# Performance work log

Hardware: AMD Instinct MI355X
Metric: run time of the kernel (lower is better)

## Reference

```python
import jax, jax.numpy as jnp
import numpy as np

ENC_IN = 64
D_MODEL = 512
B, T = 256, 256


def setup_inputs() -> dict:
    key = jax.random.key(0)
    ks = jax.random.split(key, 16)
    d = D_MODEL
    std = 1.0 / np.sqrt(d)
    def w(k, shape):
        return jax.random.normal(k, shape, dtype=jnp.float32) * std
    return {
        'x': jax.random.normal(ks[0], (B, T, ENC_IN), dtype=jnp.float32),
        'Wa': w(ks[1], (d, 2 * d)),
        'Ua': w(ks[2], (d, 2 * d)),
        'ba': jnp.zeros((2 * d,), jnp.float32),
        'Wna': w(ks[3], (d, d)),
        'Una': w(ks[4], (d, d)),
        'bna': jnp.zeros((d,), jnp.float32),
        'WAttn': w(ks[5], (d, d)),
        'UAttn': w(ks[6], (d, d)),
        'VAttn': w(ks[7], (d, d)),
        'Wma': w(ks[8], (d, d)),
        'Uma': w(ks[9], (d, d)),
        'bma': jax.random.normal(ks[10], (d,), dtype=jnp.float32),  # bias init torch.randn, dim==1 so not re-initialized
        'Wm': w(ks[11], (ENC_IN, 2 * d)),
        'Um': w(ks[12], (d, 2 * d)),
        'bm': jnp.zeros((2 * d,), jnp.float32),
        'Whm': w(ks[13], (ENC_IN, d)),
        'Uhm': w(ks[14], (d, d)),
        'bhm': jnp.zeros((d,), jnp.float32),
    }


def reference(x, Wa, Ua, ba, Wna, Una, bna, WAttn, UAttn, VAttn,
              Wma, Uma, bma, Wm, Um, bm, Whm, Uhm, bhm):
    Bsz = x.shape[0]
    H = Wna.shape[0]

    def step(carry, x_t):
        h, N, h_pp = carry           # h = h_{t-1}, h_pp = h_{t-2}
        d_t = h - h_pp               # 0 at t=0, h_0 at t=1, diff otherwise
        gates_A = d_t @ Wa + N @ Ua + ba
        z_A = jax.nn.sigmoid(gates_A[:, :H])
        r_A = jax.nn.sigmoid(gates_A[:, H:])
        hat_N = jnp.tanh(d_t @ Wna + (N * r_A) @ Una + bna)
        N_new = (1.0 - z_A) * N + z_A * hat_N
        score = jnp.tanh(h @ WAttn + N_new @ UAttn) @ VAttn
        alpha = jax.nn.softmax(score, axis=1)
        Omega = alpha * N_new
        m = jnp.tanh(Omega @ Wma + h @ Uma + bma)
        gates_M = x_t @ Wm + m @ Um + bm
        z_M = jax.nn.sigmoid(gates_M[:, :H])
        r_M = jax.nn.sigmoid(gates_M[:, H:])
        hat_h = jnp.tanh(x_t @ Whm + (m * r_M) @ Uhm + bhm)
        h_new = (1.0 - z_M) * h + z_M * hat_h
        return (h_new, N_new, h), h_new

    h0 = jnp.zeros((Bsz, H), x.dtype)
    init = (h0, h0, h0)
    (h_T, N_T, _), hs = jax.lax.scan(step, init, jnp.swapaxes(x, 0, 1))  # hs: [T,B,H]
    hidden_seq = jnp.swapaxes(hs, 0, 1)  # [B,T,H]
    return hidden_seq, (h_T, N_T)
```

## Files before the change

### kernel.cpp

```cpp
#include <hip/hip_runtime.h>

static constexpr int Bsz  = 256;
static constexpr int Tseq = 256;
static constexpr int Hd   = 512;
static constexpr int Ein  = 64;
static constexpr int NBLK = 256;
static constexpr int NTHR = 512;

typedef __attribute__((ext_vector_type(8))) short bf16x8;
typedef __attribute__((ext_vector_type(4))) float f32x4;
typedef __attribute__((ext_vector_type(8))) _Float16 f16x8;
typedef unsigned long long u64;

__device__ __forceinline__ float sigm(float x) { return 1.f / (1.f + expf(-x)); }
__device__ __forceinline__ short f2bf(float f) {
  union { float f; unsigned u; } v; v.f = f;
  unsigned r = v.u + 0x7FFFu + ((v.u >> 16) & 1u);
  return (short)(r >> 16);
}
__device__ __forceinline__ float bf2f(short s) {
  union { float f; unsigned u; } v; v.u = ((unsigned)(unsigned short)s) << 16; return v.f;
}

__device__ __forceinline__ void llc_ld8h(f16x8& d, const _Float16* p) {
  asm volatile("global_load_dwordx4 %0, %1, off sc0 sc1" : "=v"(d) : "v"(p));
}
__device__ __forceinline__ void llc_sth(_Float16* p, _Float16 v) {
  asm volatile("global_store_short %0, %1, off sc0 sc1" :: "v"(p), "v"(v) : "memory");
}
__device__ __forceinline__ void vwait() {
  asm volatile("s_waitcnt vmcnt(0)" ::: "memory");
  __builtin_amdgcn_sched_barrier(0);
}

struct KP {
  const float *x, *ba, *bna, *bma, *bm, *bhm;
  const short *Wh[13], *Wl[13];
  _Float16 *Hbuf, *Nst, *NrA, *s1, *score, *mbuf, *mrM;
  float* out;
  unsigned* cnt;
};

__global__ __launch_bounds__(256)
void prepack(const float* __restrict__ W, short* __restrict__ Whi,
             short* __restrict__ Wlo, int N)
{
  __shared__ float lds[32][257];
  const int tid = threadIdx.x;
  const int k0 = blockIdx.y * 32;
  const int n0 = blockIdx.x * 256;
  #pragma unroll
  for (int i = 0; i < 8; ++i) {
    const int flat = (i * 256 + tid) * 4;
    const int r = flat >> 8, c = flat & 255;
    const float4 v = *(const float4*)(W + (size_t)(k0 + r) * N + n0 + c);
    lds[r][c] = v.x; lds[r][c + 1] = v.y; lds[r][c + 2] = v.z; lds[r][c + 3] = v.w;
  }
  __syncthreads();
  const int lane = tid & 63, wv = tid >> 6;
  const int kr = (lane >> 4) * 8;
  const int cc = lane & 15;
  for (int nt = wv; nt < 16; nt += 4) {
    const int ntg = (n0 >> 4) + nt;
    const size_t off = ((size_t)((k0 >> 5) * (N >> 4) + ntg) * 64 + lane) * 8;
    bf16x8 vh, vl;
    #pragma unroll
    for (int j = 0; j < 8; ++j) {
      const float v = lds[kr + j][nt * 16 + cc];
      const short hb = f2bf(v);
      vh[j] = hb; vl[j] = f2bf(v - bf2f(hb));
    }
    *(bf16x8*)(Whi + off) = vh;
    *(bf16x8*)(Wlo + off) = vl;
  }
}

__device__ __forceinline__ void task_write(int task, f32x4 u0, f32x4 u1,
                                           short* hi, short* lo) {
  const int o = task << 3;
  bf16x8 vh, vl;
  #pragma unroll
  for (int j = 0; j < 4; ++j) {
    const short h0 = f2bf(u0[j]); vh[j]     = h0; vl[j]     = f2bf(u0[j] - bf2f(h0));
    const short h1 = f2bf(u1[j]); vh[j + 4] = h1; vl[j + 4] = f2bf(u1[j] - bf2f(h1));
  }
  *(bf16x8*)(hi + o) = vh;
  *(bf16x8*)(lo + o) = vl;
}
__device__ __forceinline__ void h2f8(f16x8 v, f32x4& a0, f32x4& a1) {
  #pragma unroll
  for (int j = 0; j < 4; ++j) { a0[j] = (float)v[j]; a1[j] = (float)v[j + 4]; }
}

__device__ __forceinline__ void stageSlice(const _Float16* src, short* hi, short* lo,
                                           int wid, int lane) {
  f16x8 a, b;
  llc_ld8h(a, src + (wid << 9) + (lane << 3));
  llc_ld8h(b, src + ((wid + 8) << 9) + (lane << 3));
  vwait();
  const int tb = ((lane >> 2) << 6) | ((lane & 3) << 4);
  f32x4 a0, a1, b0, b1;
  h2f8(a, a0, a1); h2f8(b, b0, b1);
  task_write(tb | wid, a0, a1, hi, lo);
  task_write(tb | (wid + 8), b0, b1, hi, lo);
}

__device__ __forceinline__ void mm(const short* Ah, const short* Al,
                                   const short* __restrict__ Wh,
                                   const short* __restrict__ Wl,
                                   int ntN, int ntg, int kc0, int kc1,
                                   int lane, f32x4& acc)
{
  for (int kc = kc0; kc < kc1; ++kc) {
    const int ao = ((kc << 6) | lane) << 3;
    const bf16x8 ah = *(const bf16x8*)(Ah + ao);
    const bf16x8 al = *(const bf16x8*)(Al + ao);
    const size_t o = ((size_t)((kc * ntN + ntg) << 6 | lane)) << 3;
    const bf16x8 bh = *(const bf16x8*)(Wh + o);
    const bf16x8 bl = *(const bf16x8*)(Wl + o);
    acc = __builtin_amdgcn_mfma_f32_16x16x32_bf16(ah, bh, acc, 0, 0, 0);
    acc = __builtin_amdgcn_mfma_f32_16x16x32_bf16(al, bh, acc, 0, 0, 0);
    acc = __builtin_amdgcn_mfma_f32_16x16x32_bf16(ah, bl, acc, 0, 0, 0);
  }
}

__device__ __forceinline__ void gbar(unsigned* cnt, int stripe, unsigned& ph) {
  asm volatile("s_waitcnt vmcnt(0)" ::: "memory");
  __syncthreads();
  ++ph;
  if (threadIdx.x == 0) {
    __hip_atomic_fetch_add(&cnt[stripe << 4], 1u, __ATOMIC_RELAXED,
                           __HIP_MEMORY_SCOPE_AGENT);
    const unsigned tgt = ph * 16u;
    while (__hip_atomic_load(&cnt[stripe << 4], __ATOMIC_RELAXED,
                             __HIP_MEMORY_SCOPE_AGENT) < tgt)
      __builtin_amdgcn_s_sleep(4);
  }
  __syncthreads();
}

__global__ __launch_bounds__(NTHR, 1)
void dtgru(KP P)
{
  __shared__ short sAh[8192], sAl[8192];
  __shared__ short sBh[8192], sBl[8192];
  __shared__ short sCh[8192], sCl[8192];
  __shared__ short sDh[8192], sDl[8192];
  __shared__ short sXh[1024], sXl[1024];
  __shared__ float red[2048];
  const int tid = threadIdx.x, lane = tid & 63, wid = tid >> 6;
  const int bid = blockIdx.x;
  const int g = bid & 15;
  const int stripe = bid >> 4;
  const int r0 = stripe << 4;
  const int nt = wid & 1;
  const int q  = wid >> 1;
  const int mat  = (wid >> 1) & 1;
  const int half = wid >> 2;
  const int ntb = (g << 1) | nt;
  const int col5 = (g << 5) | (nt << 4) | (lane & 15);
  const int rb = r0 + ((lane >> 4) << 2);
  unsigned ph = 0;
  float Nreg[4] = {0,0,0,0}, hreg[4] = {0,0,0,0};
  float zAreg[4] = {0,0,0,0}, zMreg[4] = {0,0,0,0}, mreg[4] = {0,0,0,0};
  const float b_az = P.ba[col5],  b_ar = P.ba[col5 + 512];
  const float b_na = P.bna[col5], b_ma = P.bma[col5];
  const float b_mz = P.bm[col5],  b_mr = P.bm[col5 + 512];
  const float b_hm = P.bhm[col5];

  for (int i = tid; i < 2048; i += NTHR) {
    ((u64*)sBh)[i] = 0; ((u64*)sBl)[i] = 0;
    ((u64*)sDh)[i] = 0; ((u64*)sDl)[i] = 0;
  }
  __syncthreads();

  #pragma clang loop unroll(disable)
  for (int t = 0; t < Tseq; ++t) {
    {
      const _Float16* Hr = P.Hbuf + (r0 << 9);
      f16x8 ha, hb;
      llc_ld8h(ha, Hr + (wid << 9) + (lane << 3));
      llc_ld8h(hb, Hr + ((wid + 8) << 9) + (lane << 3));
      f32x4 x0 = {0,0,0,0}, x1 = {0,0,0,0};
      if (tid < 128) {
        const float* px = P.x + ((size_t)(r0 + (tid >> 3)) * Tseq + t) * Ein
                        + ((tid & 7) << 3);
        x0 = *(const f32x4*)px; x1 = *(const f32x4*)(px + 4);
      }
      vwait();
      const int tb = ((lane >> 2) << 6) | ((lane & 3) << 4);
      auto p1w = [&](int task, f16x8 hv) {
        const int o = task << 3;
        f32x4 u0, u1; h2f8(hv, u0, u1);
        const bf16x8 dh = *(const bf16x8*)(sDh + o), dlo = *(const bf16x8*)(sDl + o);
        f32x4 d0, d1;
        #pragma unroll
        for (int j = 0; j < 4; ++j) {
          d0[j] = u0[j] - (bf2f(dh[j])     + bf2f(dlo[j]));
          d1[j] = u1[j] - (bf2f(dh[j + 4]) + bf2f(dlo[j + 4]));
        }
        task_write(task, d0, d1, sAh, sAl);
        task_write(task, u0, u1, sDh, sDl);
      };
      p1w(tb | wid, ha);
      p1w(tb | (wid + 8), hb);
      if (tid < 128) {
        const int tx = (((tid & 7) >> 2) << 6) | (tid >> 3) | ((tid & 3) << 4);
        task_write(tx, x0, x1, sXh, sXl);
      }
    }
    __syncthreads();
    {
      f32x4 acc = {0,0,0,0};
      const int ntg = (half ? 32 : 0) | ((g << 1) | nt);
      if (!mat) mm(sAh, sAl, P.Wh[0], P.Wl[0], 64, ntg, 0, 16, lane, acc);
      else      mm(sBh, sBl, P.Wh[1], P.Wl[1], 64, ntg, 0, 16, lane, acc);
      if (mat) *(f32x4*)&red[(((half << 1) | nt) << 8) | (lane << 2)] = acc;
      __syncthreads();
      if (!mat) acc += *(f32x4*)&red[(((half << 1) | nt) << 8) | (lane << 2)];
      __syncthreads();
      if (!mat && half) *(f32x4*)&red[(nt << 8) | (lane << 2)] = acc;
      __syncthreads();
      if (!mat && !half) {
        const f32x4 ar = *(const f32x4*)&red[(nt << 8) | (lane << 2)];
        #pragma unroll
        for (int i = 0; i < 4; ++i) {
          zAreg[i] = sigm(acc[i] + b_az);
          const float rA = sigm(ar[i] + b_ar);
          llc_sth(&P.NrA[((rb + i) << 9) | col5], (_Float16)(Nreg[i] * rA));
        }
      }
    }
    gbar(P.cnt, stripe, ph);

    stageSlice(P.NrA + (r0 << 9), sBh, sBl, wid, lane);
    __syncthreads();
    {
      f32x4 acc = {0,0,0,0};
      const int kc0 = (q & 1) << 3;
      if (!(q >> 1)) mm(sAh, sAl, P.Wh[2], P.Wl[2], 32, ntb, kc0, kc0 + 8, lane, acc);
      else           mm(sBh, sBl, P.Wh[3], P.Wl[3], 32, ntb, kc0, kc0 + 8, lane, acc);
      if (q) *(f32x4*)&red[((((q - 1) << 1) | nt) << 8) | (lane << 2)] = acc;
      __syncthreads();
      if (!q) {
        #pragma unroll
        for (int j = 0; j < 3; ++j) acc += *(f32x4*)&red[(((j << 1) | nt) << 8) | (lane << 2)];
        #pragma unroll
        for (int i = 0; i < 4; ++i) {
          const float hn = tanhf(acc[i] + b_na);
          const float Nn = (1.f - zAreg[i]) * Nreg[i] + zAreg[i] * hn;
          Nreg[i] = Nn;
          llc_sth(&P.Nst[((rb + i) << 9) | col5], (_Float16)Nn);
        }
      }
    }
    gbar(P.cnt, stripe, ph);

    stageSlice(P.Nst + (r0 << 9), sBh, sBl, wid, lane);
    __syncthreads();
    {
      f32x4 acc = {0,0,0,0};
      const int kc0 = (q & 1) << 3;
      if (!(q >> 1)) mm(sDh, sDl, P.Wh[4], P.Wl[4], 32, ntb, kc0, kc0 + 8, lane, acc);
      else           mm(sBh, sBl, P.Wh[5], P.Wl[5], 32, ntb, kc0, kc0 + 8, lane, acc);
      if (q) *(f32x4*)&red[((((q - 1) << 1) | nt) << 8) | (lane << 2)] = acc;
      __syncthreads();
      if (!q) {
        #pragma unroll
        for (int j = 0; j < 3; ++j) acc += *(f32x4*)&red[(((j << 1) | nt) << 8) | (lane << 2)];
        #pragma unroll
        for (int i = 0; i < 4; ++i)
          llc_sth(&P.s1[((rb + i) << 9) | col5], (_Float16)tanhf(acc[i]));
      }
    }
    gbar(P.cnt, stripe, ph);

    stageSlice(P.s1 + (r0 << 9), sCh, sCl, wid, lane);
    __syncthreads();
    {
      f32x4 acc = {0,0,0,0};
      mm(sCh, sCl, P.Wh[6], P.Wl[6], 32, ntb, q << 2, (q << 2) + 4, lane, acc);
      if (q) *(f32x4*)&red[((((q - 1) << 1) | nt) << 8) | (lane << 2)] = acc;
      __syncthreads();
      if (!q) {
        #pragma unroll
        for (int j = 0; j < 3; ++j) acc += *(f32x4*)&red[(((j << 1) | nt) << 8) | (lane << 2)];
        #pragma unroll
        for (int i = 0; i < 4; ++i)
          llc_sth(&P.score[((rb + i) << 9) | col5], (_Float16)acc[i]);
      }
    }
    gbar(P.cnt, stripe, ph);

    {
      const int lr0 = wid << 1;
      f16x8 s0v, s1v;
      llc_ld8h(s0v, P.score + ((r0 + lr0) << 9) + (lane << 3));
      llc_ld8h(s1v, P.score + ((r0 + lr0 + 1) << 9) + (lane << 3));
      vwait();
      #pragma unroll
      for (int rr = 0; rr < 2; ++rr) {
        const int lr = lr0 | rr;
        f32x4 v0, v1; h2f8(rr ? s1v : s0v, v0, v1);
        float mx = v0[0];
        #pragma unroll
        for (int j = 1; j < 4; ++j) mx = fmaxf(mx, v0[j]);
        #pragma unroll
        for (int j = 0; j < 4; ++j) mx = fmaxf(mx, v1[j]);
        #pragma unroll
        for (int d = 1; d < 64; d <<= 1) mx = fmaxf(mx, __shfl_xor(mx, d));
        float e[8];
        #pragma unroll
        for (int j = 0; j < 4; ++j) { e[j] = expf(v0[j] - mx); e[j + 4] = expf(v1[j] - mx); }
        float sm = ((e[0] + e[1]) + (e[2] + e[3])) + ((e[4] + e[5]) + (e[6] + e[7]));
        #pragma unroll
        for (int d = 1; d < 64; d <<= 1) sm += __shfl_xor(sm, d);
        const float inv = 1.f / sm;
        const int o = (((lane >> 2) << 6) | lr | ((lane & 3) << 4)) << 3;
        const bf16x8 nh = *(const bf16x8*)(sBh + o), nl = *(const bf16x8*)(sBl + o);
        bf16x8 vh, vl;
        #pragma unroll
        for (int j = 0; j < 8; ++j) {
          const float om = e[j] * inv * (bf2f(nh[j]) + bf2f(nl[j]));
          const short hb = f2bf(om);
          vh[j] = hb; vl[j] = f2bf(om - bf2f(hb));
        }
        *(bf16x8*)(sCh + o) = vh;
        *(bf16x8*)(sCl + o) = vl;
      }
    }
    __syncthreads();
    {
      f32x4 acc = {0,0,0,0};
      const int kc0 = (q & 1) << 3;
      if (!(q >> 1)) mm(sCh, sCl, P.Wh[7], P.Wl[7], 32, ntb, kc0, kc0 + 8, lane, acc);
      else           mm(sDh, sDl, P.Wh[8], P.Wl[8], 32, ntb, kc0, kc0 + 8, lane, acc);
      if (q) *(f32x4*)&red[((((q - 1) << 1) | nt) << 8) | (lane << 2)] = acc;
      __syncthreads();
      if (!q) {
        #pragma unroll
        for (int j = 0; j < 3; ++j) acc += *(f32x4*)&red[(((j << 1) | nt) << 8) | (lane << 2)];
        #pragma unroll
        for (int i = 0; i < 4; ++i) {
          const float m = tanhf(acc[i] + b_ma);
          mreg[i] = m;
          llc_sth(&P.mbuf[((rb + i) << 9) | col5], (_Float16)m);
        }
      }
    }
    gbar(P.cnt, stripe, ph);

    stageSlice(P.mbuf + (r0 << 9), sAh, sAl, wid, lane);
    __syncthreads();
    {
      f32x4 acc = {0,0,0,0};
      const int ntg = (half ? 32 : 0) | ((g << 1) | nt);
      if (!mat) { mm(sXh, sXl, P.Wh[9],  P.Wl[9],  64, ntg, 0, 2, lane, acc);
                  mm(sAh, sAl, P.Wh[10], P.Wl[10], 64, ntg, 0, 7, lane, acc); }
      else      { mm(sAh, sAl, P.Wh[10], P.Wl[10], 64, ntg, 7, 16, lane, acc); }
      if (mat) *(f32x4*)&red[(((half << 1) | nt) << 8) | (lane << 2)] = acc;
      __syncthreads();
      if (!mat) acc += *(f32x4*)&red[(((half << 1) | nt) << 8) | (lane << 2)];
      __syncthreads();
      if (!mat && half) *(f32x4*)&red[(nt << 8) | (lane << 2)] = acc;
      __syncthreads();
      if (!mat && !half) {
        const f32x4 ar = *(const f32x4*)&red[(nt << 8) | (lane << 2)];
        #pragma unroll
        for (int i = 0; i < 4; ++i) {
          zMreg[i] = sigm(acc[i] + b_mz);
          const float rM = sigm(ar[i] + b_mr);
          llc_sth(&P.mrM[((rb + i) << 9) | col5], (_Float16)(mreg[i] * rM));
        }
      }
    }
    gbar(P.cnt, stripe, ph);

    stageSlice(P.mrM + (r0 << 9), sCh, sCl, wid, lane);
    __syncthreads();
    {
      f32x4 acc = {0,0,0,0};
      if (q == 0)      { mm(sXh, sXl, P.Wh[11], P.Wl[11], 32, ntb, 0, 2, lane, acc);
                         mm(sCh, sCl, P.Wh[12], P.Wl[12], 32, ntb, 0, 2, lane, acc); }
      else if (q == 1)   mm(sCh, sCl, P.Wh[12], P.Wl[12], 32, ntb, 2, 7, lane, acc);
      else if (q == 2)   mm(sCh, sCl, P.Wh[12], P.Wl[12], 32, ntb, 7, 12, lane, acc);
      else               mm(sCh, sCl, P.Wh[12], P.Wl[12], 32, ntb, 12, 16, lane, acc);
      if (q) *(f32x4*)&red[((((q - 1) << 1) | nt) << 8) | (lane << 2)] = acc;
      __syncthreads();
      if (!q) {
        #pragma unroll
        for (int j = 0; j < 3; ++j) acc += *(f32x4*)&red[(((j << 1) | nt) << 8) | (lane << 2)];
        #pragma unroll
        for (int i = 0; i < 4; ++i) {
          const float hh = tanhf(acc[i] + b_hm);
          const float hn = (1.f - zMreg[i]) * hreg[i] + zMreg[i] * hh;
          hreg[i] = hn;
          llc_sth(&P.Hbuf[((rb + i) << 9) | col5], (_Float16)hn);
          P.out[((((size_t)(rb + i)) << 8 | t) << 9) | col5] = hn;
        }
      }
    }
    gbar(P.cnt, stripe, ph);
  }
}

__global__ __launch_bounds__(256)
void initk(_Float16* hbuf, unsigned* cnt) {
  const int i = blockIdx.x * 256 + threadIdx.x;
  hbuf[i] = (_Float16)0.f;
  if (blockIdx.x == 0) cnt[threadIdx.x] = 0u;
}

__global__ __launch_bounds__(256)
void finalize(const _Float16* __restrict__ hT, const _Float16* __restrict__ nT,
              float* __restrict__ oh, float* __restrict__ on) {
  const int i = blockIdx.x * 256 + threadIdx.x;
  unsigned a, b;
  asm volatile("global_load_ushort %0, %1, off sc0 sc1" : "=v"(a) : "v"(&hT[i]));
  asm volatile("global_load_ushort %0, %1, off sc0 sc1" : "=v"(b) : "v"(&nT[i]));
  vwait();
  unsigned short ua = (unsigned short)a, ub = (unsigned short)b;
  _Float16 ha, hb;
  __builtin_memcpy(&ha, &ua, 2); __builtin_memcpy(&hb, &ub, 2);
  oh[i] = (float)ha; on[i] = (float)hb;
}

extern "C" void kernel_launch(void* const* d_in, const int* in_sizes, int n_in,
                              void* d_out, int out_size, void* d_ws, size_t ws_size,
                              hipStream_t stream)
{
  (void)in_sizes; (void)n_in; (void)out_size; (void)ws_size;

  unsigned* cnt = (unsigned*)d_ws;
  _Float16* hw = (_Float16*)((unsigned*)d_ws + 256);
  const int S = Bsz * Hd;

  KP P{};
  P.x   = (const float*)d_in[0];
  P.ba  = (const float*)d_in[3];
  P.bna = (const float*)d_in[6];
  P.bma = (const float*)d_in[12];
  P.bm  = (const float*)d_in[15];
  P.bhm = (const float*)d_in[18];
  P.Hbuf = hw;          P.Nst = hw + S;      P.NrA = hw + 2 * S;
  P.s1   = hw + 3 * S;  P.score = hw + 4 * S;
  P.mbuf = hw + 5 * S;  P.mrM = hw + 6 * S;
  P.out = (float*)d_out;
  P.cnt = cnt;
  float* out_hT = P.out + (size_t)Bsz * Tseq * Hd;
  float* out_NT = out_hT + S;

  short* wpk = (short*)(hw + 7 * S);
  const int widx[13] = {1, 2, 4, 5, 7, 8, 9, 10, 11, 13, 14, 16, 17};
  const int wK[13]   = {512, 512, 512, 512, 512, 512, 512, 512, 512, 64, 512, 64, 512};
  const int wN[13]   = {1024, 1024, 512, 512, 512, 512, 512, 512, 512, 1024, 1024, 512, 512};
  {
    size_t off = 0;
    for (int i = 0; i < 13; ++i) {
      const size_t sz = (size_t)wK[i] * wN[i];
      P.Wh[i] = wpk + off; off += sz;
      P.Wl[i] = wpk + off; off += sz;
    }
  }
  for (int i = 0; i < 13; ++i) {
    dim3 gg(wN[i] / 256, wK[i] / 32);
    prepack<<<gg, 256, 0, stream>>>((const float*)d_in[widx[i]],
                                    (short*)P.Wh[i], (short*)P.Wl[i], wN[i]);
  }

  initk<<<S / 256, 256, 0, stream>>>(P.Hbuf, cnt);

  dtgru<<<NBLK, NTHR, 0, stream>>>(P);

  finalize<<<S / 256, 256, 0, stream>>>(P.Hbuf, P.Nst, out_hT, out_NT);
}
```

Before: 18.19 ms.

## Halve rows per block and double grid to 512 persistent blocks

Each block now processes 8 batch rows instead of 16, so the grid doubles to 512 blocks (32 stripes of 16), and launch bounds allow several blocks per CU. Shared memory is merged into one array and its size shrinks. Upper MFMA rows read a zero region, and stores from those rows are masked. The aim is more parallelism and more blocks resident per CU for the latency-bound recurrent loop. In exchange, half of each MFMA is wasted on padding, weight reads per useful row double, and twice as many stripe barriers are needed.

```diff
diff --git a/kernel.cpp b/kernel.cpp
--- a/kernel.cpp
+++ b/kernel.cpp
@@ -4,13 +4,17 @@
 static constexpr int Tseq = 256;
 static constexpr int Hd   = 512;
 static constexpr int Ein  = 64;
-static constexpr int NBLK = 256;
+static constexpr int NBLK = 512;
 static constexpr int NTHR = 512;
 
 typedef __attribute__((ext_vector_type(8))) short bf16x8;
 typedef __attribute__((ext_vector_type(4))) float f32x4;
 typedef __attribute__((ext_vector_type(8))) _Float16 f16x8;
 typedef unsigned long long u64;
+
+static constexpr int OAh = 0,     OBh = 8192,  OCh = 16384, ODh = 24576;
+static constexpr int OXh = 32768, OZ = 33792;
+static constexpr int SSZ = 34304;
 
 __device__ __forceinline__ float sigm(float x) { return 1.f / (1.f + expf(-x)); }
 __device__ __forceinline__ short f2bf(float f) {
@@ -75,46 +79,45 @@
   }
 }
 
-__device__ __forceinline__ void task_write(int task, f32x4 u0, f32x4 u1,
-                                           short* hi, short* lo) {
-  const int o = task << 3;
+__device__ __forceinline__ int to8(int r, int lane) {
+  return ((((lane >> 2) << 5) | r | ((lane & 3) << 3)) << 3);
+}
+__device__ __forceinline__ void task_write8(short* S, int base, int lo, int o,
+                                            f32x4 u0, f32x4 u1) {
   bf16x8 vh, vl;
   #pragma unroll
   for (int j = 0; j < 4; ++j) {
     const short h0 = f2bf(u0[j]); vh[j]     = h0; vl[j]     = f2bf(u0[j] - bf2f(h0));
     const short h1 = f2bf(u1[j]); vh[j + 4] = h1; vl[j + 4] = f2bf(u1[j] - bf2f(h1));
   }
-  *(bf16x8*)(hi + o) = vh;
-  *(bf16x8*)(lo + o) = vl;
+  *(bf16x8*)(S + base + o) = vh;
+  *(bf16x8*)(S + base + lo + o) = vl;
 }
 __device__ __forceinline__ void h2f8(f16x8 v, f32x4& a0, f32x4& a1) {
   #pragma unroll
   for (int j = 0; j < 4; ++j) { a0[j] = (float)v[j]; a1[j] = (float)v[j + 4]; }
 }
 
-__device__ __forceinline__ void stageSlice(const _Float16* src, short* hi, short* lo,
-                                           int wid, int lane) {
-  f16x8 a, b;
+__device__ __forceinline__ void stageSlice(short* S, int base,
+                                           const _Float16* src, int wid, int lane) {
+  f16x8 a;
   llc_ld8h(a, src + (wid << 9) + (lane << 3));
-  llc_ld8h(b, src + ((wid + 8) << 9) + (lane << 3));
   vwait();
-  const int tb = ((lane >> 2) << 6) | ((lane & 3) << 4);
-  f32x4 a0, a1, b0, b1;
-  h2f8(a, a0, a1); h2f8(b, b0, b1);
-  task_write(tb | wid, a0, a1, hi, lo);
-  task_write(tb | (wid + 8), b0, b1, hi, lo);
-}
-
-__device__ __forceinline__ void mm(const short* Ah, const short* Al,
+  f32x4 a0, a1; h2f8(a, a0, a1);
+  task_write8(S, base, 4096, to8(wid, lane), a0, a1);
+}
+
+__device__ __forceinline__ void mm(const short* S, int abase, int lo,
                                    const short* __restrict__ Wh,
                                    const short* __restrict__ Wl,
                                    int ntN, int ntg, int kc0, int kc1,
                                    int lane, f32x4& acc)
 {
+  const bool zr = (lane & 8) != 0;
   for (int kc = kc0; kc < kc1; ++kc) {
-    const int ao = ((kc << 6) | lane) << 3;
-    const bf16x8 ah = *(const bf16x8*)(Ah + ao);
-    const bf16x8 al = *(const bf16x8*)(Al + ao);
+    const int rel = (((kc << 5) | (lane & 7) | ((lane >> 4) << 3)) << 3);
+    const bf16x8 ah = *(const bf16x8*)(S + (zr ? OZ : abase + rel));
+    const bf16x8 al = *(const bf16x8*)(S + (zr ? OZ : abase + lo + rel));
     const size_t o = ((size_t)((kc * ntN + ntg) << 6 | lane)) << 3;
     const bf16x8 bh = *(const bf16x8*)(Wh + o);
     const bf16x8 bl = *(const bf16x8*)(Wl + o);
@@ -139,20 +142,16 @@
   __syncthreads();
 }
 
-__global__ __launch_bounds__(NTHR, 1)
+__global__ __launch_bounds__(NTHR, 4)
 void dtgru(KP P)
 {
-  __shared__ short sAh[8192], sAl[8192];
-  __shared__ short sBh[8192], sBl[8192];
-  __shared__ short sCh[8192], sCl[8192];
-  __shared__ short sDh[8192], sDl[8192];
-  __shared__ short sXh[1024], sXl[1024];
-  __shared__ float red[2048];
+  __shared__ short S[SSZ];
+  __shared__ float red[1536];
   const int tid = threadIdx.x, lane = tid & 63, wid = tid >> 6;
   const int bid = blockIdx.x;
   const int g = bid & 15;
   const int stripe = bid >> 4;
-  const int r0 = stripe << 4;
+  const int r0 = stripe << 3;
   const int nt = wid & 1;
   const int q  = wid >> 1;
   const int mat  = (wid >> 1) & 1;
@@ -160,6 +159,7 @@
   const int ntb = (g << 1) | nt;
   const int col5 = (g << 5) | (nt << 4) | (lane & 15);
   const int rb = r0 + ((lane >> 4) << 2);
+  const bool rowok = lane < 32;
   unsigned ph = 0;
   float Nreg[4] = {0,0,0,0}, hreg[4] = {0,0,0,0};
   float zAreg[4] = {0,0,0,0}, zMreg[4] = {0,0,0,0}, mreg[4] = {0,0,0,0};
@@ -168,53 +168,47 @@
   const float b_mz = P.bm[col5],  b_mr = P.bm[col5 + 512];
   const float b_hm = P.bhm[col5];
 
-  for (int i = tid; i < 2048; i += NTHR) {
-    ((u64*)sBh)[i] = 0; ((u64*)sBl)[i] = 0;
-    ((u64*)sDh)[i] = 0; ((u64*)sDl)[i] = 0;
-  }
+  for (int i = tid; i < SSZ / 4; i += NTHR) ((u64*)S)[i] = 0;
   __syncthreads();
 
   #pragma clang loop unroll(disable)
   for (int t = 0; t < Tseq; ++t) {
     {
       const _Float16* Hr = P.Hbuf + (r0 << 9);
-      f16x8 ha, hb;
+      f16x8 ha;
       llc_ld8h(ha, Hr + (wid << 9) + (lane << 3));
-      llc_ld8h(hb, Hr + ((wid + 8) << 9) + (lane << 3));
       f32x4 x0 = {0,0,0,0}, x1 = {0,0,0,0};
-      if (tid < 128) {
+      if (tid < 64) {
         const float* px = P.x + ((size_t)(r0 + (tid >> 3)) * Tseq + t) * Ein
                         + ((tid & 7) << 3);
         x0 = *(const f32x4*)px; x1 = *(const f32x4*)(px + 4);
       }
       vwait();
-      const int tb = ((lane >> 2) << 6) | ((lane & 3) << 4);
-      auto p1w = [&](int task, f16x8 hv) {
-        const int o = task << 3;
-        f32x4 u0, u1; h2f8(hv, u0, u1);
-        const bf16x8 dh = *(const bf16x8*)(sDh + o), dlo = *(const bf16x8*)(sDl + o);
+      {
+        const int o = to8(wid, lane);
+        f32x4 u0, u1; h2f8(ha, u0, u1);
+        const bf16x8 dh = *(const bf16x8*)(S + ODh + o);
+        const bf16x8 dl = *(const bf16x8*)(S + ODh + 4096 + o);
         f32x4 d0, d1;
         #pragma unroll
         for (int j = 0; j < 4; ++j) {
-          d0[j] = u0[j] - (bf2f(dh[j])     + bf2f(dlo[j]));
-          d1[j] = u1[j] - (bf2f(dh[j + 4]) + bf2f(dlo[j + 4]));
-        }
-        task_write(task, d0, d1, sAh, sAl);
-        task_write(task, u0, u1, sDh, sDl);
-      };
-      p1w(tb | wid, ha);
-      p1w(tb | (wid + 8), hb);
-      if (tid < 128) {
-        const int tx = (((tid & 7) >> 2) << 6) | (tid >> 3) | ((tid & 3) << 4);
-        task_write(tx, x0, x1, sXh, sXl);
+          d0[j] = u0[j] - (bf2f(dh[j])     + bf2f(dl[j]));
+          d1[j] = u1[j] - (bf2f(dh[j + 4]) + bf2f(dl[j + 4]));
+        }
+        task_write8(S, OAh, 4096, o, d0, d1);
+        task_write8(S, ODh, 4096, o, u0, u1);
+      }
+      if (tid < 64) {
+        const int ox = (((((tid >> 2) & 1) << 5) | (tid >> 3) | ((tid & 3) << 3)) << 3);
+        task_write8(S, OXh, 512, ox, x0, x1);
       }
     }
     __syncthreads();
     {
       f32x4 acc = {0,0,0,0};
       const int ntg = (half ? 32 : 0) | ((g << 1) | nt);
-      if (!mat) mm(sAh, sAl, P.Wh[0], P.Wl[0], 64, ntg, 0, 16, lane, acc);
-      else      mm(sBh, sBl, P.Wh[1], P.Wl[1], 64, ntg, 0, 16, lane, acc);
+      if (!mat) mm(S, OAh, 4096, P.Wh[0], P.Wl[0], 64, ntg, 0, 16, lane, acc);
+      else      mm(S, OBh, 4096, P.Wh[1], P.Wl[1], 64, ntg, 0, 16, lane, acc);
       if (mat) *(f32x4*)&red[(((half << 1) | nt) << 8) | (lane << 2)] = acc;
       __syncthreads();
       if (!mat) acc += *(f32x4*)&red[(((half << 1) | nt) << 8) | (lane << 2)];
@@ -227,19 +221,19 @@
         for (int i = 0; i < 4; ++i) {
           zAreg[i] = sigm(acc[i] + b_az);
           const float rA = sigm(ar[i] + b_ar);
-          llc_sth(&P.NrA[((rb + i) << 9) | col5], (_Float16)(Nreg[i] * rA));
-        }
-      }
-    }
-    gbar(P.cnt, stripe, ph);
-
-    stageSlice(P.NrA + (r0 << 9), sBh, sBl, wid, lane);
+          if (rowok) llc_sth(&P.NrA[((rb + i) << 9) | col5], (_Float16)(Nreg[i] * rA));
+        }
+      }
+    }
+    gbar(P.cnt, stripe, ph);
+
+    stageSlice(S, OBh, P.NrA + (r0 << 9), wid, lane);
     __syncthreads();
     {
       f32x4 acc = {0,0,0,0};
       const int kc0 = (q & 1) << 3;
-      if (!(q >> 1)) mm(sAh, sAl, P.Wh[2], P.Wl[2], 32, ntb, kc0, kc0 + 8, lane, acc);
-      else           mm(sBh, sBl, P.Wh[3], P.Wl[3], 32, ntb, kc0, kc0 + 8, lane, acc);
+      if (!(q >> 1)) mm(S, OAh, 4096, P.Wh[2], P.Wl[2], 32, ntb, kc0, kc0 + 8, lane, acc);
+      else           mm(S, OBh, 4096, P.Wh[3], P.Wl[3], 32, ntb, kc0, kc0 + 8, lane, acc);
       if (q) *(f32x4*)&red[((((q - 1) << 1) | nt) << 8) | (lane << 2)] = acc;
       __syncthreads();
       if (!q) {
@@ -250,19 +244,19 @@
           const float hn = tanhf(acc[i] + b_na);
           const float Nn = (1.f - zAreg[i]) * Nreg[i] + zAreg[i] * hn;
           Nreg[i] = Nn;
-          llc_sth(&P.Nst[((rb + i) << 9) | col5], (_Float16)Nn);
-        }
-      }
-    }
-    gbar(P.cnt, stripe, ph);
-
-    stageSlice(P.Nst + (r0 << 9), sBh, sBl, wid, lane);
+          if (rowok) llc_sth(&P.Nst[((rb + i) << 9) | col5], (_Float16)Nn);
+        }
+      }
+    }
+    gbar(P.cnt, stripe, ph);
+
+    stageSlice(S, OBh, P.Nst + (r0 << 9), wid, lane);
     __syncthreads();
     {
       f32x4 acc = {0,0,0,0};
       const int kc0 = (q & 1) << 3;
-      if (!(q >> 1)) mm(sDh, sDl, P.Wh[4], P.Wl[4], 32, ntb, kc0, kc0 + 8, lane, acc);
-      else           mm(sBh, sBl, P.Wh[5], P.Wl[5], 32, ntb, kc0, kc0 + 8, lane, acc);
+      if (!(q >> 1)) mm(S, ODh, 4096, P.Wh[4], P.Wl[4], 32, ntb, kc0, kc0 + 8, lane, acc);
+      else           mm(S, OBh, 4096, P.Wh[5], P.Wl[5], 32, ntb, kc0, kc0 + 8, lane, acc);
       if (q) *(f32x4*)&red[((((q - 1) << 1) | nt) << 8) | (lane << 2)] = acc;
       __syncthreads();
       if (!q) {
@@ -270,16 +264,16 @@
         for (int j = 0; j < 3; ++j) acc += *(f32x4*)&red[(((j << 1) | nt) << 8) | (lane << 2)];
         #pragma unroll
         for (int i = 0; i < 4; ++i)
-          llc_sth(&P.s1[((rb + i) << 9) | col5], (_Float16)tanhf(acc[i]));
-      }
-    }
-    gbar(P.cnt, stripe, ph);
-
-    stageSlice(P.s1 + (r0 << 9), sCh, sCl, wid, lane);
-    __syncthreads();
-    {
-      f32x4 acc = {0,0,0,0};
-      mm(sCh, sCl, P.Wh[6], P.Wl[6], 32, ntb, q << 2, (q << 2) + 4, lane, acc);
+          if (rowok) llc_sth(&P.s1[((rb + i) << 9) | col5], (_Float16)tanhf(acc[i]));
+      }
+    }
+    gbar(P.cnt, stripe, ph);
+
+    stageSlice(S, OCh, P.s1 + (r0 << 9), wid, lane);
+    __syncthreads();
+    {
+      f32x4 acc = {0,0,0,0};
+      mm(S, OCh, 4096, P.Wh[6], P.Wl[6], 32, ntb, q << 2, (q << 2) + 4, lane, acc);
       if (q) *(f32x4*)&red[((((q - 1) << 1) | nt) << 8) | (lane << 2)] = acc;
       __syncthreads();
       if (!q) {
@@ -287,54 +281,47 @@
         for (int j = 0; j < 3; ++j) acc += *(f32x4*)&red[(((j << 1) | nt) << 8) | (lane << 2)];
         #pragma unroll
         for (int i = 0; i < 4; ++i)
-          llc_sth(&P.score[((rb + i) << 9) | col5], (_Float16)acc[i]);
-      }
-    }
-    gbar(P.cnt, stripe, ph);
-
-    {
-      const int lr0 = wid << 1;
-      f16x8 s0v, s1v;
-      llc_ld8h(s0v, P.score + ((r0 + lr0) << 9) + (lane << 3));
-      llc_ld8h(s1v, P.score + ((r0 + lr0 + 1) << 9) + (lane << 3));
+          if (rowok) llc_sth(&P.score[((rb + i) << 9) | col5], (_Float16)acc[i]);
+      }
+    }
+    gbar(P.cnt, stripe, ph);
+
+    {
+      f16x8 sv;
+      llc_ld8h(sv, P.score + ((r0 + wid) << 9) + (lane << 3));
       vwait();
-      #pragma unroll
-      for (int rr = 0; rr < 2; ++rr) {
-        const int lr = lr0 | rr;
-        f32x4 v0, v1; h2f8(rr ? s1v : s0v, v0, v1);
-        float mx = v0[0];
-        #pragma unroll
-        for (int j = 1; j < 4; ++j) mx = fmaxf(mx, v0[j]);
-        #pragma unroll
-        for (int j = 0; j < 4; ++j) mx = fmaxf(mx, v1[j]);
-        #pragma unroll
-        for (int d = 1; d < 64; d <<= 1) mx = fmaxf(mx, __shfl_xor(mx, d));
-        float e[8];
-        #pragma unroll
-        for (int j = 0; j < 4; ++j) { e[j] = expf(v0[j] - mx); e[j + 4] = expf(v1[j] - mx); }
-        float sm = ((e[0] + e[1]) + (e[2] + e[3])) + ((e[4] + e[5]) + (e[6] + e[7]));
-        #pragma unroll
-        for (int d = 1; d < 64; d <<= 1) sm += __shfl_xor(sm, d);
-        const float inv = 1.f / sm;
-        const int o = (((lane >> 2) << 6) | lr | ((lane & 3) << 4)) << 3;
-        const bf16x8 nh = *(const bf16x8*)(sBh + o), nl = *(const bf16x8*)(sBl + o);
-        bf16x8 vh, vl;
-        #pragma unroll
-        for (int j = 0; j < 8; ++j) {
-          const float om = e[j] * inv * (bf2f(nh[j]) + bf2f(nl[j]));
-          const short hb = f2bf(om);
-          vh[j] = hb; vl[j] = f2bf(om - bf2f(hb));
-        }
-        *(bf16x8*)(sCh + o) = vh;
-        *(bf16x8*)(sCl + o) = vl;
-      }
+      f32x4 v0, v1; h2f8(sv, v0, v1);
+      float mx = v0[0];
+      #pragma unroll
+      for (int j = 1; j < 4; ++j) mx = fmaxf(mx, v0[j]);
+      #pragma unroll
+      for (int j = 0; j < 4; ++j) mx = fmaxf(mx, v1[j]);
+      #pragma unroll
+      for (int d = 1; d < 64; d <<= 1) mx = fmaxf(mx, __shfl_xor(mx, d));
+      float e[8];
+      #pragma unroll
+      for (int j = 0; j < 4; ++j) { e[j] = expf(v0[j] - mx); e[j + 4] = expf(v1[j] - mx); }
+      float sm = ((e[0] + e[1]) + (e[2] + e[3])) + ((e[4] + e[5]) + (e[6] + e[7]));
+      #pragma unroll
+      for (int d = 1; d < 64; d <<= 1) sm += __shfl_xor(sm, d);
+      const float inv = 1.f / sm;
+      const int o = to8(wid, lane);
+      const bf16x8 nh = *(const bf16x8*)(S + OBh + o);
+      const bf16x8 nl = *(const bf16x8*)(S + OBh + 4096 + o);
+      f32x4 w0, w1;
+      #pragma unroll
+      for (int j = 0; j < 4; ++j) {
+        w0[j] = e[j]     * inv * (bf2f(nh[j])     + bf2f(nl[j]));
+        w1[j] = e[j + 4] * inv * (bf2f(nh[j + 4]) + bf2f(nl[j + 4]));
+      }
+      task_write8(S, OCh, 4096, o, w0, w1);
     }
     __syncthreads();
     {
       f32x4 acc = {0,0,0,0};
       const int kc0 = (q & 1) << 3;
-      if (!(q >> 1)) mm(sCh, sCl, P.Wh[7], P.Wl[7], 32, ntb, kc0, kc0 + 8, lane, acc);
-      else           mm(sDh, sDl, P.Wh[8], P.Wl[8], 32, ntb, kc0, kc0 + 8, lane, acc);
+      if (!(q >> 1)) mm(S, OCh, 4096, P.Wh[7], P.Wl[7], 32, ntb, kc0, kc0 + 8, lane, acc);
+      else           mm(S, ODh, 4096, P.Wh[8], P.Wl[8], 32, ntb, kc0, kc0 + 8, lane, acc);
       if (q) *(f32x4*)&red[((((q - 1) << 1) | nt) << 8) | (lane << 2)] = acc;
       __syncthreads();
       if (!q) {
@@ -344,20 +331,20 @@
         for (int i = 0; i < 4; ++i) {
           const float m = tanhf(acc[i] + b_ma);
           mreg[i] = m;
-          llc_sth(&P.mbuf[((rb + i) << 9) | col5], (_Float16)m);
-        }
-      }
-    }
-    gbar(P.cnt, stripe, ph);
-
-    stageSlice(P.mbuf + (r0 << 9), sAh, sAl, wid, lane);
+          if (rowok) llc_sth(&P.mbuf[((rb + i) << 9) | col5], (_Float16)m);
+        }
+      }
+    }
+    gbar(P.cnt, stripe, ph);
+
+    stageSlice(S, OAh, P.mbuf + (r0 << 9), wid, lane);
     __syncthreads();
     {
       f32x4 acc = {0,0,0,0};
       const int ntg = (half ? 32 : 0) | ((g << 1) | nt);
-      if (!mat) { mm(sXh, sXl, P.Wh[9],  P.Wl[9],  64, ntg, 0, 2, lane, acc);
-                  mm(sAh, sAl, P.Wh[10], P.Wl[10], 64, ntg, 0, 7, lane, acc); }
-      else      { mm(sAh, sAl, P.Wh[10], P.Wl[10], 64, ntg, 7, 16, lane, acc); }
+      if (!mat) { mm(S, OXh, 512,  P.Wh[9],  P.Wl[9],  64, ntg, 0, 2, lane, acc);
+                  mm(S, OAh, 4096, P.Wh[10], P.Wl[10], 64, ntg, 0, 7, lane, acc); }
+      else      { mm(S, OAh, 4096, P.Wh[10], P.Wl[10], 64, ntg, 7, 16, lane, acc); }
       if (mat) *(f32x4*)&red[(((half << 1) | nt) << 8) | (lane << 2)] = acc;
       __syncthreads();
       if (!mat) acc += *(f32x4*)&red[(((half << 1) | nt) << 8) | (lane << 2)];
@@ -370,21 +357,21 @@
         for (int i = 0; i < 4; ++i) {
           zMreg[i] = sigm(acc[i] + b_mz);
           const float rM = sigm(ar[i] + b_mr);
-          llc_sth(&P.mrM[((rb + i) << 9) | col5], (_Float16)(mreg[i] * rM));
-        }
-      }
-    }
-    gbar(P.cnt, stripe, ph);
-
-    stageSlice(P.mrM + (r0 << 9), sCh, sCl, wid, lane);
-    __syncthreads();
-    {
-      f32x4 acc = {0,0,0,0};
-      if (q == 0)      { mm(sXh, sXl, P.Wh[11], P.Wl[11], 32, ntb, 0, 2, lane, acc);
-                         mm(sCh, sCl, P.Wh[12], P.Wl[12], 32, ntb, 0, 2, lane, acc); }
-      else if (q == 1)   mm(sCh, sCl, P.Wh[12], P.Wl[12], 32, ntb, 2, 7, lane, acc);
-      else if (q == 2)   mm(sCh, sCl, P.Wh[12], P.Wl[12], 32, ntb, 7, 12, lane, acc);
-      else               mm(sCh, sCl, P.Wh[12], P.Wl[12], 32, ntb, 12, 16, lane, acc);
+          if (rowok) llc_sth(&P.mrM[((rb + i) << 9) | col5], (_Float16)(mreg[i] * rM));
+        }
+      }
+    }
+    gbar(P.cnt, stripe, ph);
+
+    stageSlice(S, OCh, P.mrM + (r0 << 9), wid, lane);
+    __syncthreads();
+    {
+      f32x4 acc = {0,0,0,0};
+      if (q == 0)      { mm(S, OXh, 512,  P.Wh[11], P.Wl[11], 32, ntb, 0, 2, lane, acc);
+                         mm(S, OCh, 4096, P.Wh[12], P.Wl[12], 32, ntb, 0, 2, lane, acc); }
+      else if (q == 1)   mm(S, OCh, 4096, P.Wh[12], P.Wl[12], 32, ntb, 2, 7, lane, acc);
+      else if (q == 2)   mm(S, OCh, 4096, P.Wh[12], P.Wl[12], 32, ntb, 7, 12, lane, acc);
+      else               mm(S, OCh, 4096, P.Wh[12], P.Wl[12], 32, ntb, 12, 16, lane, acc);
       if (q) *(f32x4*)&red[((((q - 1) << 1) | nt) << 8) | (lane << 2)] = acc;
       __syncthreads();
       if (!q) {
@@ -395,8 +382,10 @@
           const float hh = tanhf(acc[i] + b_hm);
           const float hn = (1.f - zMreg[i]) * hreg[i] + zMreg[i] * hh;
           hreg[i] = hn;
-          llc_sth(&P.Hbuf[((rb + i) << 9) | col5], (_Float16)hn);
-          P.out[((((size_t)(rb + i)) << 8 | t) << 9) | col5] = hn;
+          if (rowok) {
+            llc_sth(&P.Hbuf[((rb + i) << 9) | col5], (_Float16)hn);
+            P.out[((((size_t)(rb + i)) << 8 | t) << 9) | col5] = hn;
+          }
         }
       }
     }
@@ -408,7 +397,7 @@
 void initk(_Float16* hbuf, unsigned* cnt) {
   const int i = blockIdx.x * 256 + threadIdx.x;
   hbuf[i] = (_Float16)0.f;
-  if (blockIdx.x == 0) cnt[threadIdx.x] = 0u;
+  if (blockIdx.x < 2) cnt[blockIdx.x * 256 + threadIdx.x] = 0u;
 }
 
 __global__ __launch_bounds__(256)
@@ -432,7 +421,7 @@
   (void)in_sizes; (void)n_in; (void)out_size; (void)ws_size;
 
   unsigned* cnt = (unsigned*)d_ws;
-  _Float16* hw = (_Float16*)((unsigned*)d_ws + 256);
+  _Float16* hw = (_Float16*)((unsigned*)d_ws + 1024);
   const int S = Bsz * Hd;
 
   KP P{};
```

Result: slower. 35.48 ms (+95.0%).
